# Optimization experiments

Measured on AMD Instinct MI355X. Metric: run time of the kernel, lower is better.

The kernel has to match this reference:

```python
import jax, jax.numpy as jnp
import numpy as np

B, T, D = 64, 8192, 128
UNITS = 128

def setup_inputs() -> dict:
    key = jax.random.key(0)
    k1, k2, k3 = jax.random.split(key, 3)
    inputs = jax.random.normal(k1, (B, T, D), dtype=jnp.float32)
    # Dense(units): kernel [D, units], bias [units]
    W_kernel = jax.random.normal(k2, (D, UNITS), dtype=jnp.float32) * (1.0 / np.sqrt(D))
    W_bias = jnp.zeros((UNITS,), dtype=jnp.float32)
    # Dense(1): kernel [units, 1], bias [1]
    V_kernel = jax.random.normal(k3, (UNITS, 1), dtype=jnp.float32) * (1.0 / np.sqrt(UNITS))
    V_bias = jnp.zeros((1,), dtype=jnp.float32)
    return {"inputs": inputs, "W_kernel": W_kernel, "W_bias": W_bias,
            "V_kernel": V_kernel, "V_bias": V_bias}

def reference(inputs, W_kernel, W_bias, V_kernel, V_bias):
    # score: [B, T, units]
    score = jnp.tanh(jnp.einsum('btd,du->btu', inputs, W_kernel) + W_bias)
    # logits: [B, T, 1]; softmax over time axis (axis=1)
    logits = jnp.einsum('btu,uo->bto', score, V_kernel) + V_bias
    attention_weights = jax.nn.softmax(logits, axis=1)
    # weighted sum over time -> [B, D]
    context_vector = jnp.sum(attention_weights * inputs, axis=1)
    return context_vector
```

## Files before the change

kernel.cpp:

```cpp
#include <hip/hip_runtime.h>
#include <hip/hip_bf16.h>

typedef __attribute__((ext_vector_type(8))) short short8;
typedef __attribute__((ext_vector_type(4))) float f32x4;

#define B_SZ 64
#define T_SZ 8192
#define D_SZ 128
#define U_SZ 128
#define T_TILE 64
#define GRID_P 1024
#define TILES_PER_BLK 8
#define P_STRIDE 132
#define WT_LD 136

__device__ __forceinline__ unsigned short f2bf(float f) {
  unsigned int u = __builtin_bit_cast(unsigned int, f);
  u += 0x7fffu + ((u >> 16) & 1u);
  return (unsigned short)(u >> 16);
}

__device__ __forceinline__ float bf2f(unsigned short s) {
  return __builtin_bit_cast(float, (unsigned int)s << 16);
}

__device__ __forceinline__ float fast_tanh(float x) {
  float e = __expf(2.0f * x);
  return 1.0f - 2.0f * __builtin_amdgcn_rcpf(e + 1.0f);
}

template<int CTRL>
__device__ __forceinline__ float dpp_add(float v) {
  int t = __builtin_amdgcn_update_dpp(0, __builtin_bit_cast(int, v),
                                      CTRL, 0xf, 0xf, true);
  return v + __builtin_bit_cast(float, t);
}
__device__ __forceinline__ float row_reduce16(float v) {
  v = dpp_add<0x118>(v);
  v = dpp_add<0x114>(v);
  v = dpp_add<0x112>(v);
  v = dpp_add<0x111>(v);
  return v;
}

__device__ __forceinline__ void cvt_tile(const float4 pf[8], short8 afrag[4]) {
#pragma unroll
  for (int kt = 0; kt < 4; ++kt) {
    short8 a;
#pragma unroll
    for (int j = 0; j < 4; ++j) {
      float4 f = pf[kt * 2 + (j >> 1)];
      a[j * 2]     = (short)f2bf(j & 1 ? f.z : f.x);
      a[j * 2 + 1] = (short)f2bf(j & 1 ? f.w : f.y);
    }
    afrag[kt] = a;
  }
}

__global__ void k_prep(const float* __restrict__ wk, unsigned short* __restrict__ wt) {
  int i = blockIdx.x * 256 + threadIdx.x;
  if (i < D_SZ * U_SZ) {
    int d = i >> 7, u = i & 127;
    wt[u * D_SZ + d] = f2bf(wk[i]);
  }
}

__global__ __launch_bounds__(256) void k_partial(
    const float* __restrict__ x, const unsigned short* __restrict__ wt_g,
    const float* __restrict__ wb, const float* __restrict__ v,
    const float* __restrict__ vb, float* __restrict__ pbuf)
{
  __shared__ unsigned short wt[U_SZ][WT_LD];
  __shared__ float wb_s[U_SZ], v_s[U_SZ];
  __shared__ float logits[4][16];
  __shared__ float fin[4][D_SZ];
  __shared__ float fm[4], fs[4];

  const int tid  = threadIdx.x;
  const int bidx = blockIdx.x;

  for (int i = tid; i < U_SZ * 16; i += 256) {
    int row = i >> 4, c16 = i & 15;
    uint4 val = ((const uint4*)wt_g)[i];
    *(uint4*)&wt[row][c16 * 8] = val;
  }
  if (tid < U_SZ) { wb_s[tid] = wb[tid]; v_s[tid] = v[tid]; }
  __syncthreads();

  const int w  = tid >> 6;
  const int l  = tid & 63;
  const int lr = l & 15;
  const int lh = l >> 4;
  const float vbias = vb[0];

  const int b        = bidx >> 4;
  const int row0     = (bidx & 15) * (TILES_PER_BLK * T_TILE);
  const float* xbase = x + ((size_t)b * T_SZ + row0 + w * 16 + lr) * D_SZ + lh * 8;

  float4 pf[8];
#pragma unroll
  for (int kt = 0; kt < 4; ++kt) {
    pf[kt * 2]     = *(const float4*)(xbase + kt * 32);
    pf[kt * 2 + 1] = *(const float4*)(xbase + kt * 32 + 4);
  }
  short8 afrag[4];
  cvt_tile(pf, afrag);

  float m_run = -3.0e38f, s_run = 0.0f;
  float rc[4][8];
#pragma unroll
  for (int kt = 0; kt < 4; ++kt)
#pragma unroll
    for (int j = 0; j < 8; ++j) rc[kt][j] = 0.0f;

  for (int it = 0; it < TILES_PER_BLK; ++it) {
    if (it + 1 < TILES_PER_BLK) {
      const float* p = xbase + (size_t)(it + 1) * T_TILE * D_SZ;
#pragma unroll
      for (int kt = 0; kt < 4; ++kt) {
        pf[kt * 2]     = *(const float4*)(p + kt * 32);
        pf[kt * 2 + 1] = *(const float4*)(p + kt * 32 + 4);
      }
      __builtin_amdgcn_sched_barrier(0);
    }

    float lg[4] = {0.f, 0.f, 0.f, 0.f};
#pragma unroll
    for (int ut = 0; ut < 8; ++ut) {
      f32x4 acc = {0.f, 0.f, 0.f, 0.f};
#pragma unroll
      for (int kt = 0; kt < 4; ++kt) {
        short8 bfrag = *(const short8*)&wt[ut * 16 + lr][kt * 32 + lh * 8];
        acc = __builtin_amdgcn_mfma_f32_16x16x32_bf16(afrag[kt], bfrag, acc, 0, 0, 0);
      }
      const float wbv = wb_s[ut * 16 + lr];
      const float vv  = v_s[ut * 16 + lr];
#pragma unroll
      for (int r = 0; r < 4; ++r)
        lg[r] += fast_tanh(acc[r] + wbv) * vv;
    }
#pragma unroll
    for (int r = 0; r < 4; ++r) lg[r] = row_reduce16(lg[r]);
    if (lr == 15) {
#pragma unroll
      for (int r = 0; r < 4; ++r)
        logits[w][lh * 4 + r] = lg[r] + vbias;
    }

    float lv = logits[w][lr];
    float mx = lv;
#pragma unroll
    for (int k = 1; k <= 8; k <<= 1) mx = fmaxf(mx, __shfl_xor(mx, k, 64));
    const float m_new = fmaxf(m_run, mx);
    const float e_old = __expf(m_run - m_new);
    const float pr    = __expf(lv - m_new);
    float ss = pr;
#pragma unroll
    for (int k = 1; k <= 8; k <<= 1) ss += __shfl_xor(ss, k, 64);
    s_run = s_run * e_old + ss;
    m_run = m_new;

#pragma unroll
    for (int kt = 0; kt < 4; ++kt) {
#pragma unroll
      for (int j = 0; j < 8; ++j) {
        rc[kt][j] = fmaf(rc[kt][j], e_old,
                         pr * bf2f((unsigned short)afrag[kt][j]));
      }
    }

    __builtin_amdgcn_sched_barrier(0);
    if (it + 1 < TILES_PER_BLK) cvt_tile(pf, afrag);
  }

  if (l == 0) { fm[w] = m_run; fs[w] = s_run; }
  __syncthreads();
  const float m_blk = fmaxf(fmaxf(fm[0], fm[1]), fmaxf(fm[2], fm[3]));
  const float e_w   = __expf(m_run - m_blk);
#pragma unroll
  for (int kt = 0; kt < 4; ++kt) {
    float cs[8];
#pragma unroll
    for (int j = 0; j < 8; ++j) cs[j] = row_reduce16(rc[kt][j]);
    if (lr == 15) {
      f32x4 v0 = {cs[0] * e_w, cs[1] * e_w, cs[2] * e_w, cs[3] * e_w};
      f32x4 v1 = {cs[4] * e_w, cs[5] * e_w, cs[6] * e_w, cs[7] * e_w};
      *(f32x4*)&fin[w][kt * 32 + lh * 8]     = v0;
      *(f32x4*)&fin[w][kt * 32 + lh * 8 + 4] = v1;
    }
  }
  __syncthreads();

  float* pb = pbuf + (size_t)bidx * P_STRIDE;
  if (tid < 128) {
    pb[tid] = fin[0][tid] + fin[1][tid] + fin[2][tid] + fin[3][tid];
  } else if (tid == 128) {
    pb[128] = m_blk;
  } else if (tid == 129) {
    float sb = fs[0] * __expf(fm[0] - m_blk) + fs[1] * __expf(fm[1] - m_blk)
             + fs[2] * __expf(fm[2] - m_blk) + fs[3] * __expf(fm[3] - m_blk);
    pb[129] = sb;
  }
}

__global__ __launch_bounds__(128) void k_combine(const float* __restrict__ pbuf,
                                                 float* __restrict__ out)
{
  const int b = blockIdx.x, tid = threadIdx.x;
  __shared__ float sm[16], sden[16];
  const float* base = pbuf + (size_t)b * 16 * P_STRIDE;

  if (tid < 16) {
    sm[tid]   = base[tid * P_STRIDE + 128];
    sden[tid] = base[tid * P_STRIDE + 129];
  }
  __syncthreads();

  float mx = -3.0e38f;
#pragma unroll
  for (int i = 0; i < 16; ++i) mx = fmaxf(mx, sm[i]);
  float den = 0.0f, c = 0.0f;
#pragma unroll
  for (int i = 0; i < 16; ++i) {
    float e = __expf(sm[i] - mx);
    den += sden[i] * e;
    c = fmaf(base[(size_t)i * P_STRIDE + tid], e, c);
  }
  out[b * D_SZ + tid] = c / den;
}

extern "C" void kernel_launch(void* const* d_in, const int* in_sizes, int n_in,
                              void* d_out, int out_size, void* d_ws, size_t ws_size,
                              hipStream_t stream) {
  const float* x  = (const float*)d_in[0];
  const float* wk = (const float*)d_in[1];
  const float* wb = (const float*)d_in[2];
  const float* vk = (const float*)d_in[3];
  const float* vb = (const float*)d_in[4];
  float* out = (float*)d_out;

  unsigned short* wt = (unsigned short*)d_ws;
  float* pbuf = (float*)((char*)d_ws + 32768);

  k_prep<<<64, 256, 0, stream>>>(wk, wt);
  k_partial<<<GRID_P, 256, 0, stream>>>(x, wt, wb, vk, vb, pbuf);
  k_combine<<<B_SZ, 128, 0, stream>>>(pbuf, out);
}
```

Measured before the change: 63.86 us.

## Double the grid, issue first x loads before weight staging, use nontemporal loads

Halves the tiles each block processes so the grid doubles to 2048 blocks, and the combine kernel now merges 32 partials per batch. The first tile's input loads are moved ahead of the shared-memory weight staging so global latency overlaps with the weight copy. All input loads become nontemporal since x is streamed once. The trade-off is more blocks, each redoing the weight staging and the partial writes, plus a larger combine step.

Result: slower. 75.30 us (+17.9%).

```diff
diff --git a/kernel.cpp b/kernel.cpp
--- a/kernel.cpp
+++ b/kernel.cpp
@@ -9,8 +9,9 @@
 #define D_SZ 128
 #define U_SZ 128
 #define T_TILE 64
-#define GRID_P 1024
-#define TILES_PER_BLK 8
+#define GRID_P 2048
+#define TILES_PER_BLK 4
+#define BLKS_PER_B 32
 #define P_STRIDE 132
 #define WT_LD 136
 
@@ -43,15 +44,15 @@
   return v;
 }
 
-__device__ __forceinline__ void cvt_tile(const float4 pf[8], short8 afrag[4]) {
+__device__ __forceinline__ void cvt_tile(const f32x4 pf[8], short8 afrag[4]) {
 #pragma unroll
   for (int kt = 0; kt < 4; ++kt) {
     short8 a;
 #pragma unroll
     for (int j = 0; j < 4; ++j) {
-      float4 f = pf[kt * 2 + (j >> 1)];
-      a[j * 2]     = (short)f2bf(j & 1 ? f.z : f.x);
-      a[j * 2 + 1] = (short)f2bf(j & 1 ? f.w : f.y);
+      f32x4 f = pf[kt * 2 + (j >> 1)];
+      a[j * 2]     = (short)f2bf(j & 1 ? f[2] : f[0]);
+      a[j * 2 + 1] = (short)f2bf(j & 1 ? f[3] : f[1]);
     }
     afrag[kt] = a;
   }
@@ -79,6 +80,23 @@
   const int tid  = threadIdx.x;
   const int bidx = blockIdx.x;
 
+  const int w  = tid >> 6;
+  const int l  = tid & 63;
+  const int lr = l & 15;
+  const int lh = l >> 4;
+
+  const int b        = bidx >> 5;
+  const int row0     = (bidx & (BLKS_PER_B - 1)) * (TILES_PER_BLK * T_TILE);
+  const float* xbase = x + ((size_t)b * T_SZ + row0 + w * 16 + lr) * D_SZ + lh * 8;
+
+  f32x4 pf[8];
+#pragma unroll
+  for (int kt = 0; kt < 4; ++kt) {
+    pf[kt * 2]     = __builtin_nontemporal_load((const f32x4*)(xbase + kt * 32));
+    pf[kt * 2 + 1] = __builtin_nontemporal_load((const f32x4*)(xbase + kt * 32 + 4));
+  }
+  __builtin_amdgcn_sched_barrier(0);
+
   for (int i = tid; i < U_SZ * 16; i += 256) {
     int row = i >> 4, c16 = i & 15;
     uint4 val = ((const uint4*)wt_g)[i];
@@ -87,22 +105,7 @@
   if (tid < U_SZ) { wb_s[tid] = wb[tid]; v_s[tid] = v[tid]; }
   __syncthreads();
 
-  const int w  = tid >> 6;
-  const int l  = tid & 63;
-  const int lr = l & 15;
-  const int lh = l >> 4;
   const float vbias = vb[0];
-
-  const int b        = bidx >> 4;
-  const int row0     = (bidx & 15) * (TILES_PER_BLK * T_TILE);
-  const float* xbase = x + ((size_t)b * T_SZ + row0 + w * 16 + lr) * D_SZ + lh * 8;
-
-  float4 pf[8];
-#pragma unroll
-  for (int kt = 0; kt < 4; ++kt) {
-    pf[kt * 2]     = *(const float4*)(xbase + kt * 32);
-    pf[kt * 2 + 1] = *(const float4*)(xbase + kt * 32 + 4);
-  }
   short8 afrag[4];
   cvt_tile(pf, afrag);
 
@@ -118,8 +121,8 @@
       const float* p = xbase + (size_t)(it + 1) * T_TILE * D_SZ;
 #pragma unroll
       for (int kt = 0; kt < 4; ++kt) {
-        pf[kt * 2]     = *(const float4*)(p + kt * 32);
-        pf[kt * 2 + 1] = *(const float4*)(p + kt * 32 + 4);
+        pf[kt * 2]     = __builtin_nontemporal_load((const f32x4*)(p + kt * 32));
+        pf[kt * 2 + 1] = __builtin_nontemporal_load((const f32x4*)(p + kt * 32 + 4));
       }
       __builtin_amdgcn_sched_barrier(0);
     }
@@ -207,10 +210,10 @@
                                                  float* __restrict__ out)
 {
   const int b = blockIdx.x, tid = threadIdx.x;
-  __shared__ float sm[16], sden[16];
-  const float* base = pbuf + (size_t)b * 16 * P_STRIDE;
-
-  if (tid < 16) {
+  __shared__ float sm[BLKS_PER_B], sden[BLKS_PER_B];
+  const float* base = pbuf + (size_t)b * BLKS_PER_B * P_STRIDE;
+
+  if (tid < BLKS_PER_B) {
     sm[tid]   = base[tid * P_STRIDE + 128];
     sden[tid] = base[tid * P_STRIDE + 129];
   }
@@ -218,10 +221,10 @@
 
   float mx = -3.0e38f;
 #pragma unroll
-  for (int i = 0; i < 16; ++i) mx = fmaxf(mx, sm[i]);
+  for (int i = 0; i < BLKS_PER_B; ++i) mx = fmaxf(mx, sm[i]);
   float den = 0.0f, c = 0.0f;
-#pragma unroll
-  for (int i = 0; i < 16; ++i) {
+#pragma unroll 8
+  for (int i = 0; i < BLKS_PER_B; ++i) {
     float e = __expf(sm[i] - mx);
     den += sden[i] * e;
     c = fmaf(base[(size_t)i * P_STRIDE + tid], e, c);
```
